# Kernel tuning notes

Measured on AMD Instinct MI355X. Metric: run time of the kernel, lower is better.

The kernel has to match this reference:

```python
import jax, jax.numpy as jnp
import numpy as np

B, HT_, WT_, DM, C = 32, 32, 32, 768, 64  # batch, token grid, token dim, hough channels
THETA_RES, RHO_RES = 3, 1


def hough_transform(rows, cols, theta_res, rho_res):
    """Precompute binary vote matrix [rows*cols, n_rho*n_theta] (HT-LCNN style)."""
    theta = np.linspace(0.0, 180.0, int(np.ceil(180.0 / theta_res)) + 1)[:-1]
    w = theta.size                                # n_theta
    diag = np.sqrt((rows - 1) ** 2 + (cols - 1) ** 2)
    q = int(np.ceil(diag / rho_res))
    nrho = 2 * q + 1                              # n_rho
    cos_t, sin_t = np.cos(np.deg2rad(theta)), np.sin(np.deg2rad(theta))
    ii, jj = np.meshgrid(np.arange(rows), np.arange(cols), indexing='ij')
    xc = jj - cols / 2.0                          # centered pixel coords
    yc = rows / 2.0 - ii
    rho = xc[..., None] * cos_t + yc[..., None] * sin_t   # [rows, cols, w]
    ridx = np.round(rho / rho_res).astype(np.int64) + q
    tidx = np.broadcast_to(np.arange(w), ridx.shape)
    flat = (ridx * w + tidx).reshape(rows * cols, w)      # bin = rho_idx*w + theta_idx
    vote = np.zeros((rows * cols, nrho * w), dtype=np.float32)
    vote[np.arange(rows * cols)[:, None], flat] = 1.0
    return vote, nrho, w


def setup_inputs() -> dict:
    key = jax.random.key(0)
    ks = jax.random.split(key, 8)
    vote_np, n_rho, n_theta = hough_transform(HT_, WT_, THETA_RES, RHO_RES)
    ch = C // 2
    s = lambda n: 1.0 / np.sqrt(n)
    return dict(
        tokens=jax.random.normal(ks[0], (B, HT_ * WT_, DM), jnp.float32),
        vote=jnp.asarray(vote_np),                                    # [N, HR]
        Wt_in=jax.random.normal(ks[1], (C, DM), jnp.float32) * s(DM),   # to_feats 1x1
        bt_in=jnp.zeros((C,), jnp.float32),
        W1=jax.random.normal(ks[2], (ch, C), jnp.float32) * s(C),       # conv1 1x1 (no bias)
        W2=jax.random.normal(ks[3], (ch, ch, 9, 1), jnp.float32) * s(ch * 9),  # (9,1) conv on hough map
        W3=jax.random.normal(ks[4], (C, ch), jnp.float32) * s(ch),      # conv3 1x1 (no bias)
        Wt_out=jax.random.normal(ks[5], (DM, C), jnp.float32) * s(C),   # from_feats 1x1
        bt_out=jnp.zeros((DM,), jnp.float32),
        n_rho=n_rho,
        n_theta=n_theta,
    )


def reference(tokens, vote, Wt_in, bt_in, W1, W2, W3, Wt_out, bt_out, n_rho, n_theta):
    # tokens: [B, N, D]; vote: [N, HR] with HR = n_rho * n_theta.
    # 1x1 convs over the token grid are position-independent -> plain matmuls on [B, N, *].
    norm = jnp.clip(vote.sum(0), 1.0)                       # [HR] HT vote-count normalizer
    feat = tokens @ Wt_in.T + bt_in                         # [B, N, C]   (to_feats)
    y = jax.nn.relu(feat @ W1.T)                            # [B, N, ch]  (conv1 + relu)
    # HT: relu (idempotent here) + vote gather as dense matmul, normalized per hough bin
    ht = jnp.einsum('bnc,nh->bch', y, vote) / norm          # [B, ch, HR]
    bb, ch, hr = ht.shape
    ht = ht.reshape(bb, ch, n_rho, n_theta)                 # [B, ch, n_rho, n_theta]
    ht = jax.lax.conv_general_dilated(                      # (9,1) conv along rho, pad 4
        ht, W2, (1, 1), ((4, 4), (0, 0)),
        dimension_numbers=('NCHW', 'OIHW', 'NCHW'))
    # IHT: relu + transposed vote scatter, normalized by n_theta
    iht = jnp.einsum('bch,nh->bnc', jax.nn.relu(ht.reshape(bb, ch, hr)), vote) / n_theta
    z = iht @ W3.T                                          # [B, N, C]   (conv3)
    out = (feat + z) @ Wt_out.T + bt_out                    # residual + from_feats -> [B, N, D]
    return out
```

## Files before the change

### kernel.cpp

```cpp
#include <hip/hip_runtime.h>
#include <math.h>

#define NB    32
#define NTOK  1024
#define DMODEL 768
#define CF    64
#define CHH   32
#define NRHO  89
#define NTH   60
#define HRB   (NRHO*NTH)

typedef short bf16x8 __attribute__((ext_vector_type(8)));
typedef float f32x4  __attribute__((ext_vector_type(4)));
typedef unsigned int uint;
typedef unsigned short ushort;
typedef unsigned char uchar;

__device__ __forceinline__ ushort f2bf(float f) {
    uint u = __float_as_uint(f);
    return (ushort)((u + 0x7FFF + ((u >> 16) & 1)) >> 16);
}
__device__ __forceinline__ float bf2f(ushort u) {
    return __uint_as_float(((uint)u) << 16);
}
__device__ __forceinline__ uint cvtpk(float lo, float hi) {
    uint r;
    asm("v_cvt_pk_bf16_f32 %0, %1, %2" : "=v"(r) : "v"(lo), "v"(hi));
    return r;
}

#define GLDS16(gp, lp) __builtin_amdgcn_global_load_lds( \
    (const __attribute__((address_space(1))) unsigned int*)(gp), \
    (__attribute__((address_space(3))) unsigned int*)(lp), 16, 0, 0)

__global__ __launch_bounds__(256) void k0_prep(
    int* __restrict__ perm, int* __restrict__ rowptr, uchar* __restrict__ rho8,
    const float* __restrict__ Wt_in, const float* __restrict__ bt_in,
    const float* __restrict__ W1, short* __restrict__ wcat,
    float* __restrict__ bcat,
    const float* __restrict__ Wt_out, const float* __restrict__ W2,
    short* __restrict__ wout, short* __restrict__ w2t) {
    __shared__ int rho_n[NTOK];
    __shared__ int cnt2[64 * 90];
    __shared__ int tot[96];
    __shared__ int base[96];
    __shared__ float w1row[64];
    const int tid = threadIdx.x;
    const int blk = blockIdx.x;

    if (blk < 60) {
        const int t = blk;
        const double rad = ((double)(t * 3)) * (M_PI / 180.0);
        const double ct = cos(rad), st = sin(rad);
        for (int n = tid; n < NTOK; n += 256) {
            int i = n >> 5, j = n & 31;
            double rho = (double)(j - 16) * ct + (double)(16 - i) * st;
            int ridx = (int)rint(rho) + 44;
            rho_n[n] = ridx;
            rho8[t * NTOK + n] = (uchar)ridx;
        }
        for (int i = tid; i < 64 * 90; i += 256) cnt2[i] = 0;
        __syncthreads();
        for (int n = tid; n < NTOK; n += 256)
            atomicAdd(&cnt2[(n >> 4) * 90 + rho_n[n]], 1);
        __syncthreads();
        if (tid < NRHO) {
            int s = 0;
            for (int c = 0; c < 64; ++c) {
                int v = cnt2[c * 90 + tid];
                cnt2[c * 90 + tid] = s;
                s += v;
            }
            tot[tid] = s;
        }
        __syncthreads();
        if (tid == 0) {
            int s = 0;
            for (int r = 0; r < NRHO; ++r) { base[r] = s; s += tot[r]; }
            base[NRHO] = s;
        }
        __syncthreads();
        if (tid < NRHO + 1) rowptr[t * 90 + tid] = base[tid];
        if (tid < 64) {
            const int c = tid;
            #pragma unroll
            for (int j = 0; j < 16; ++j) {
                int n = c * 16 + j;
                int r = rho_n[n];
                int cur = cnt2[c * 90 + r];
                cnt2[c * 90 + r] = cur + 1;
                perm[t * NTOK + base[r] + cur] = n;
            }
        }
    } else if (blk < 156) {
        const int c = blk - 60;
        if (c >= 64)
            for (int j = tid; j < 64; j += 256) w1row[j] = W1[(c - 64) * 64 + j];
        __syncthreads();
        for (int k = tid; k < DMODEL; k += 256) {
            float v;
            if (c < 64) v = Wt_in[c * DMODEL + k];
            else {
                v = 0.0f;
                for (int j = 0; j < 64; ++j) v += w1row[j] * Wt_in[j * DMODEL + k];
            }
            int kt = k >> 6, kk = k & 63;
            wcat[(((kt << 3) + (kk >> 3)) * 96 + c) * 8 + (k & 7)] = (short)f2bf(v);
        }
        if (tid == 0) {
            float bv;
            if (c < 64) bv = bt_in[c];
            else {
                bv = 0.0f;
                for (int j = 0; j < 64; ++j) bv += W1[(c - 64) * 64 + j] * bt_in[j];
            }
            bcat[c] = bv;
        }
    } else {
        int idx = (blk - 156) * 256 + tid;
        if (idx < 6144) {
            int d = idx >> 3, kg = idx & 7;
            float4 a = *(const float4*)&Wt_out[d * 64 + kg * 8];
            float4 b = *(const float4*)&Wt_out[d * 64 + kg * 8 + 4];
            uint4 v = make_uint4(cvtpk(a.x, a.y), cvtpk(a.z, a.w),
                                 cvtpk(b.x, b.y), cvtpk(b.z, b.w));
            *(uint4*)&wout[(((d >> 7) * 8 + kg) * 128 + (d & 127)) * 8] = v;
        } else if (idx < 6144 + 9216) {
            int q = idx - 6144;
            int e = q & 7, ln = (q >> 3) & 63, wm = (q >> 9) & 1, k = q >> 10;
            int o = wm * 16 + (ln & 15), i = ((ln >> 4) << 3) + e;
            w2t[q] = (short)f2bf(W2[(o * 32 + i) * 9 + k]);
        }
    }
}

__global__ __launch_bounds__(256) void k1_mfma(
    const float* __restrict__ tokens, const short* __restrict__ wcat,
    const float* __restrict__ bcat, ushort* __restrict__ featb,
    ushort* __restrict__ ybb) {
    __shared__ __align__(16) short Asm[2][4096];
    __shared__ __align__(16) short Bsm[2][6144];

    const int tid = threadIdx.x;
    const int lane = tid & 63, wave = tid >> 6;
    const int wm = wave >> 1, wn = wave & 1;
    const int row0 = blockIdx.x * 64;
    const int sm = tid >> 2, sq = tid & 3;

    const float* arow = tokens + (size_t)(row0 + sm) * DMODEL;

    f32x4 acc[2][3] = {};
    float4 ta[4];

    #pragma unroll
    for (int p = 0; p < 4; ++p)
        ta[p] = *(const float4*)&arow[(sq + 4 * p) * 4];
    for (int ch = tid; ch < 768; ch += 256)
        GLDS16((const char*)wcat + ch * 16, (char*)Bsm[0] + ch * 16);
    #pragma unroll
    for (int p = 0; p < 4; ++p) {
        int q = sq + 4 * p, kg = q >> 1, half = q & 1;
        uint lo = cvtpk(ta[p].x, ta[p].y);
        uint hi = cvtpk(ta[p].z, ta[p].w);
        *(uint2*)((char*)Asm[0] + (kg * 64 + sm) * 16 + half * 8) = make_uint2(lo, hi);
    }
    __syncthreads();

    int cur = 0;
    for (int kt = 0; kt < 12; ++kt) {
        if (kt < 11) {
            const float* src = arow + (kt + 1) * 64;
            #pragma unroll
            for (int p = 0; p < 4; ++p)
                ta[p] = *(const float4*)&src[(sq + 4 * p) * 4];
            const char* bsrc = (const char*)wcat + (size_t)(kt + 1) * 12288;
            for (int ch = tid; ch < 768; ch += 256)
                GLDS16(bsrc + ch * 16, (char*)Bsm[cur ^ 1] + ch * 16);
        }
        const bf16x8* Ap = (const bf16x8*)Asm[cur];
        const bf16x8* Bp = (const bf16x8*)Bsm[cur];
        #pragma unroll
        for (int ks = 0; ks < 2; ++ks) {
            int kg = (lane >> 4) + ks * 4;
            bf16x8 av[2], bv[3];
            #pragma unroll
            for (int i = 0; i < 2; ++i)
                av[i] = Ap[kg * 64 + wm * 32 + i * 16 + (lane & 15)];
            #pragma unroll
            for (int j = 0; j < 3; ++j)
                bv[j] = Bp[kg * 96 + wn * 48 + j * 16 + (lane & 15)];
            #pragma unroll
            for (int i = 0; i < 2; ++i)
                #pragma unroll
                for (int j = 0; j < 3; ++j)
                    acc[i][j] = __builtin_amdgcn_mfma_f32_16x16x32_bf16(
                        av[i], bv[j], acc[i][j], 0, 0, 0);
        }
        if (kt < 11) {
            #pragma unroll
            for (int p = 0; p < 4; ++p) {
                int q = sq + 4 * p, kg = q >> 1, half = q & 1;
                uint lo = cvtpk(ta[p].x, ta[p].y);
                uint hi = cvtpk(ta[p].z, ta[p].w);
                *(uint2*)((char*)Asm[cur ^ 1] + (kg * 64 + sm) * 16 + half * 8) =
                    make_uint2(lo, hi);
            }
        }
        __syncthreads();
        cur ^= 1;
    }

    ushort* fs = (ushort*)Asm[0];
    ushort* ys = (ushort*)Asm[1];
    float bb[3];
    #pragma unroll
    for (int j = 0; j < 3; ++j) bb[j] = bcat[wn * 48 + j * 16 + (lane & 15)];
    #pragma unroll
    for (int i = 0; i < 2; ++i) {
        #pragma unroll
        for (int j = 0; j < 3; ++j) {
            int c = wn * 48 + j * 16 + (lane & 15);
            int mlb = wm * 32 + i * 16 + ((lane >> 4) << 2);
            #pragma unroll
            for (int r = 0; r < 4; ++r) {
                float v = acc[i][j][r] + bb[j];
                if (c < 64) fs[(mlb + r) * 64 + c] = f2bf(v);
                else        ys[(mlb + r) * 32 + (c - 64)] = f2bf(fmaxf(v, 0.0f));
            }
        }
    }
    __syncthreads();
    for (int idx = tid; idx < 512; idx += 256) {
        int ml = idx >> 3, cq = (idx & 7) * 8;
        *(uint4*)&featb[(size_t)(row0 + ml) * CF + cq] = *(const uint4*)&fs[ml * 64 + cq];
    }
    {
        int ml = tid >> 2, cq = (tid & 3) * 8;
        *(uint4*)&ybb[(size_t)(row0 + ml) * CHH + cq] = *(const uint4*)&ys[ml * 32 + cq];
    }
}

__global__ __launch_bounds__(256) void k23_ht_conv(
    const ushort* __restrict__ ybb, const int* __restrict__ perm,
    const int* __restrict__ rowptr, const short* __restrict__ w2t,
    ushort* __restrict__ htcT) {
    __shared__ int pperm[NTOK];
    __shared__ int prow[90];
    __shared__ __align__(16) short insp[104 * 40];
    __shared__ uint outtu[NRHO * 18];

    const int tid = threadIdx.x;
    const int lane = tid & 63, wave = tid >> 6;
    const int wm = wave >> 1, wn = wave & 1;
    const int b = blockIdx.x / NTH, t = blockIdx.x % NTH;

    bf16x8 av[9];
    #pragma unroll
    for (int k = 0; k < 9; ++k)
        av[k] = *(const bf16x8*)&w2t[(((k * 2 + wm) * 64) + lane) * 8];

    for (int i = tid; i < NTOK; i += 256) pperm[i] = perm[t * NTOK + i];
    for (int i = tid; i < 90; i += 256) prow[i] = rowptr[t * 90 + i];
    for (int i = tid; i < 104 * 40 / 2; i += 256) ((uint*)insp)[i] = 0;
    __syncthreads();

    {
        const int c0 = (tid & 3) * 8, g = tid >> 2;
        const ushort* yp = ybb + (size_t)b * NTOK * CHH + c0;
        for (int rho = g; rho < NRHO; rho += 64) {
            int p0 = prow[rho], p1 = prow[rho + 1];
            float s0 = 0, s1 = 0, s2 = 0, s3 = 0, s4 = 0, s5 = 0, s6 = 0, s7 = 0;
            for (int k = p0; k < p1; ++k) {
                int n = pperm[k];
                uint4 v = *(const uint4*)&yp[n * CHH];
                s0 += bf2f((ushort)(v.x & 0xffff)); s1 += bf2f((ushort)(v.x >> 16));
                s2 += bf2f((ushort)(v.y & 0xffff)); s3 += bf2f((ushort)(v.y >> 16));
                s4 += bf2f((ushort)(v.z & 0xffff)); s5 += bf2f((ushort)(v.z >> 16));
                s6 += bf2f((ushort)(v.w & 0xffff)); s7 += bf2f((ushort)(v.w >> 16));
            }
            float iv = 1.0f / fmaxf((float)(p1 - p0), 1.0f);
            uint4 pk = make_uint4(cvtpk(s0 * iv, s1 * iv), cvtpk(s2 * iv, s3 * iv),
                                  cvtpk(s4 * iv, s5 * iv), cvtpk(s6 * iv, s7 * iv));
            *(uint4*)&insp[(rho + 4) * 40 + c0] = pk;
        }
    }
    __syncthreads();

    f32x4 acc[3] = {};
    #pragma unroll
    for (int f = 0; f < 3; ++f) {
        int Rn = wn * 48 + f * 16 + (lane & 15);
        #pragma unroll
        for (int k = 0; k < 9; ++k) {
            bf16x8 bv = *(const bf16x8*)&insp[(Rn + k) * 40 + ((lane >> 4) << 3)];
            acc[f] = __builtin_amdgcn_mfma_f32_16x16x32_bf16(av[k], bv, acc[f], 0, 0, 0);
        }
    }
    #pragma unroll
    for (int f = 0; f < 3; ++f) {
        int r = wn * 48 + f * 16 + (lane & 15);
        if (r < NRHO) {
            int ob = wm * 8 + ((lane >> 4) << 1);
            outtu[r * 18 + ob]     = cvtpk(fmaxf(acc[f][0], 0.0f), fmaxf(acc[f][1], 0.0f));
            outtu[r * 18 + ob + 1] = cvtpk(fmaxf(acc[f][2], 0.0f), fmaxf(acc[f][3], 0.0f));
        }
    }
    __syncthreads();

    {
        ushort* dst = htcT + (size_t)(b * NTH + t) * (NRHO * CHH);
        for (int idx = tid; idx < NRHO * 8; idx += 256) {
            int r = idx >> 3, q = idx & 7;
            uint2 v;
            v.x = outtu[r * 18 + q * 2];
            v.y = outtu[r * 18 + q * 2 + 1];
            *(uint2*)&dst[r * CHH + q * 4] = v;
        }
    }
}

__global__ __launch_bounds__(256, 4) void k45_iht_out(
    const ushort* __restrict__ htcT, const uchar* __restrict__ rho8,
    const float* __restrict__ W3, const ushort* __restrict__ featb,
    const short* __restrict__ wout, const float* __restrict__ bt_out,
    float* __restrict__ out) {
    __shared__ __align__(16) char smem[40960];
    short* Blds = (short*)smem;
    short* Alds = (short*)(smem + 32768);
    float* w3t  = (float*)smem;
    uchar* lrho = (uchar*)(smem + 8192);
    float* ihts = (float*)(smem + 12032);

    const int tid = threadIdx.x;
    const int lane = tid & 63, wave = tid >> 6;
    const int wm = wave >> 1, wn = wave & 1;
    const int bid = blockIdx.x;
    const int b = bid >> 4;
    const int n0 = (bid & 15) * 64;

    for (int idx = tid; idx < 2048; idx += 256) {
        int c = idx >> 6, j = idx & 63;
        w3t[idx] = W3[j * 32 + c];
    }
    for (int idx = tid; idx < NTH * 64; idx += 256)
        lrho[idx] = rho8[(idx >> 6) * NTOK + n0 + (idx & 63)];
    __syncthreads();

    {
        const int c0 = (tid & 3) * 8, tok = tid >> 2;
        const ushort* hb = htcT + (size_t)b * NTH * NRHO * CHH + c0;
        float s[8] = {};
        #pragma unroll 6
        for (int t = 0; t < NTH; ++t) {
            int r = lrho[t * 64 + tok];
            uint4 v = *(const uint4*)&hb[(size_t)(t * NRHO + r) * CHH];
            s[0] += bf2f((ushort)(v.x & 0xffff)); s[1] += bf2f((ushort)(v.x >> 16));
            s[2] += bf2f((ushort)(v.y & 0xffff)); s[3] += bf2f((ushort)(v.y >> 16));
            s[4] += bf2f((ushort)(v.z & 0xffff)); s[5] += bf2f((ushort)(v.z >> 16));
            s[6] += bf2f((ushort)(v.w & 0xffff)); s[7] += bf2f((ushort)(v.w >> 16));
        }
        __syncthreads();
        float4 r0, r1;
        r0.x = s[0] * (1.0f / 60.0f); r0.y = s[1] * (1.0f / 60.0f);
        r0.z = s[2] * (1.0f / 60.0f); r0.w = s[3] * (1.0f / 60.0f);
        r1.x = s[4] * (1.0f / 60.0f); r1.y = s[5] * (1.0f / 60.0f);
        r1.z = s[6] * (1.0f / 60.0f); r1.w = s[7] * (1.0f / 60.0f);
        *(float4*)&ihts[tok * 32 + c0] = r0;
        *(float4*)&ihts[tok * 32 + c0 + 4] = r1;
    }
    __syncthreads();

    {
        const int j = tid & 63, nb = tid >> 6;
        ushort* Au = (ushort*)Alds;
        for (int nn = nb; nn < 64; nn += 4) {
            float z = 0.0f;
            #pragma unroll 8
            for (int cc = 0; cc < 32; ++cc) z += ihts[nn * 32 + cc] * w3t[cc * 64 + j];
            float v = bf2f(featb[(size_t)(bid * 64 + nn) * CF + j]) + z;
            Au[((j >> 3) * 64 + nn) * 8 + (j & 7)] = f2bf(v);
        }
    }
    __syncthreads();

    for (int ch = tid; ch < 1024; ch += 256)
        GLDS16((const char*)wout + ch * 16, (char*)Blds + ch * 16);
    __syncthreads();

    const bf16x8* Ap = (const bf16x8*)Alds;
    for (int db = 0; db < 6; ++db) {
        if (db < 5) {
            const char* src = (const char*)wout + (size_t)(db + 1) * 16384;
            char* dst = (char*)Blds + ((db + 1) & 1) * 16384;
            for (int ch = tid; ch < 1024; ch += 256)
                GLDS16(src + ch * 16, dst + ch * 16);
        }
        const bf16x8* Bp = (const bf16x8*)((const char*)Blds + (db & 1) * 16384);
        f32x4 acc[2][4] = {};
        #pragma unroll
        for (int ks = 0; ks < 2; ++ks) {
            int kg = (lane >> 4) + ks * 4;
            bf16x8 avv[2], bvv[4];
            #pragma unroll
            for (int i = 0; i < 2; ++i)
                avv[i] = Ap[kg * 64 + wm * 32 + i * 16 + (lane & 15)];
            #pragma unroll
            for (int jf = 0; jf < 4; ++jf)
                bvv[jf] = Bp[kg * 128 + wn * 64 + jf * 16 + (lane & 15)];
            #pragma unroll
            for (int i = 0; i < 2; ++i)
                #pragma unroll
                for (int jf = 0; jf < 4; ++jf)
                    acc[i][jf] = __builtin_amdgcn_mfma_f32_16x16x32_bf16(
                        avv[i], bvv[jf], acc[i][jf], 0, 0, 0);
        }
        const int d0 = db * 128 + wn * 64 + (lane & 15);
        float bb[4];
        #pragma unroll
        for (int jf = 0; jf < 4; ++jf) bb[jf] = bt_out[d0 + jf * 16];
        const int mrow = bid * 64 + wm * 32 + ((lane >> 4) << 2);
        #pragma unroll
        for (int i = 0; i < 2; ++i)
            #pragma unroll
            for (int r = 0; r < 4; ++r)
                #pragma unroll
                for (int jf = 0; jf < 4; ++jf)
                    out[(size_t)(mrow + i * 16 + r) * DMODEL + d0 + jf * 16] =
                        acc[i][jf][r] + bb[jf];
        __syncthreads();
    }
}

extern "C" void kernel_launch(void* const* d_in, const int* in_sizes, int n_in,
                              void* d_out, int out_size, void* d_ws, size_t ws_size,
                              hipStream_t stream) {
    const float* tokens = (const float*)d_in[0];
    const float* Wt_in  = (const float*)d_in[2];
    const float* bt_in  = (const float*)d_in[3];
    const float* W1     = (const float*)d_in[4];
    const float* W2     = (const float*)d_in[5];
    const float* W3     = (const float*)d_in[6];
    const float* Wt_out = (const float*)d_in[7];
    const float* bt_out = (const float*)d_in[8];
    float* out = (float*)d_out;

    char* w = (char*)d_ws;
    int*    perm   = (int*)(w);
    int*    rowptr = (int*)(w + 245760);
    uchar*  rho8   = (uchar*)(w + 267360);
    short*  wcat   = (short*)(w + 328800);
    float*  bcat   = (float*)(w + 476256);
    short*  wout   = (short*)(w + 476640);
    short*  w2t    = (short*)(w + 574944);
    ushort* featb  = (ushort*)(w + 593376);
    ushort* ybb    = (ushort*)(w + 4787680);
    ushort* htcT   = (ushort*)(w + 6884832);

    k0_prep<<<216, 256, 0, stream>>>(perm, rowptr, rho8, Wt_in, bt_in, W1,
                                     wcat, bcat, Wt_out, W2, wout, w2t);
    k1_mfma<<<NB * NTOK / 64, 256, 0, stream>>>(tokens, wcat, bcat, featb, ybb);
    k23_ht_conv<<<NB * NTH, 256, 0, stream>>>(ybb, perm, rowptr, w2t, htcT);
    k45_iht_out<<<NB * (NTOK / 64), 256, 0, stream>>>(htcT, rho8, W3, featb,
                                                      wout, bt_out, out);
}
```

Measured before the change: 100.4 us.

## Load MFMA operands straight from global memory, dropping LDS staging in two GEMMs

The token projection kernel now loads fp32 activations and bf16 weights directly into registers in MFMA fragment layout instead of staging them through double-buffered LDS. It also doubles the rows per block to 128 and sets a 4-blocks-per-CU launch bound. The output GEMM likewise reads the weight fragments from global memory, keeps the A fragments in registers across all output column tiles, and removes the per-tile barriers. This cuts LDS traffic and synchronisation, but relies on L1/L2 caching for the repeated weight reads, and the uncoalesced 32-byte row reads of tokens may reduce memory efficiency.

```diff
diff --git a/kernel.cpp b/kernel.cpp
--- a/kernel.cpp
+++ b/kernel.cpp
@@ -28,10 +28,13 @@
     asm("v_cvt_pk_bf16_f32 %0, %1, %2" : "=v"(r) : "v"(lo), "v"(hi));
     return r;
 }
-
-#define GLDS16(gp, lp) __builtin_amdgcn_global_load_lds( \
-    (const __attribute__((address_space(1))) unsigned int*)(gp), \
-    (__attribute__((address_space(3))) unsigned int*)(lp), 16, 0, 0)
+__device__ __forceinline__ bf16x8 pack8(const float4& a, const float4& b) {
+    uint4 u = make_uint4(cvtpk(a.x, a.y), cvtpk(a.z, a.w),
+                         cvtpk(b.x, b.y), cvtpk(b.z, b.w));
+    union { uint4 u4; bf16x8 v; } cv;
+    cv.u4 = u;
+    return cv.v;
+}
 
 __global__ __launch_bounds__(256) void k0_prep(
     int* __restrict__ perm, int* __restrict__ rowptr, uchar* __restrict__ rho8,
@@ -134,93 +137,58 @@
     }
 }
 
-__global__ __launch_bounds__(256) void k1_mfma(
+__global__ __launch_bounds__(256, 4) void k1_mfma(
     const float* __restrict__ tokens, const short* __restrict__ wcat,
     const float* __restrict__ bcat, ushort* __restrict__ featb,
     ushort* __restrict__ ybb) {
-    __shared__ __align__(16) short Asm[2][4096];
-    __shared__ __align__(16) short Bsm[2][6144];
+    __shared__ ushort fs[128 * 64];
+    __shared__ ushort ys[128 * 32];
 
     const int tid = threadIdx.x;
     const int lane = tid & 63, wave = tid >> 6;
     const int wm = wave >> 1, wn = wave & 1;
-    const int row0 = blockIdx.x * 64;
-    const int sm = tid >> 2, sq = tid & 3;
-
-    const float* arow = tokens + (size_t)(row0 + sm) * DMODEL;
-
-    f32x4 acc[2][3] = {};
-    float4 ta[4];
-
-    #pragma unroll
-    for (int p = 0; p < 4; ++p)
-        ta[p] = *(const float4*)&arow[(sq + 4 * p) * 4];
-    for (int ch = tid; ch < 768; ch += 256)
-        GLDS16((const char*)wcat + ch * 16, (char*)Bsm[0] + ch * 16);
-    #pragma unroll
-    for (int p = 0; p < 4; ++p) {
-        int q = sq + 4 * p, kg = q >> 1, half = q & 1;
-        uint lo = cvtpk(ta[p].x, ta[p].y);
-        uint hi = cvtpk(ta[p].z, ta[p].w);
-        *(uint2*)((char*)Asm[0] + (kg * 64 + sm) * 16 + half * 8) = make_uint2(lo, hi);
-    }
-    __syncthreads();
-
-    int cur = 0;
+    const int row0 = blockIdx.x * 128;
+    const int l15 = lane & 15, lq = lane >> 4;
+
+    const float* aptr = tokens + (size_t)(row0 + wm * 64 + l15) * DMODEL + lq * 8;
+    const short* bptr = wcat + ((size_t)lq * 96 + wn * 48 + l15) * 8;
+
+    f32x4 acc[4][3] = {};
+
     for (int kt = 0; kt < 12; ++kt) {
-        if (kt < 11) {
-            const float* src = arow + (kt + 1) * 64;
-            #pragma unroll
-            for (int p = 0; p < 4; ++p)
-                ta[p] = *(const float4*)&src[(sq + 4 * p) * 4];
-            const char* bsrc = (const char*)wcat + (size_t)(kt + 1) * 12288;
-            for (int ch = tid; ch < 768; ch += 256)
-                GLDS16(bsrc + ch * 16, (char*)Bsm[cur ^ 1] + ch * 16);
-        }
-        const bf16x8* Ap = (const bf16x8*)Asm[cur];
-        const bf16x8* Bp = (const bf16x8*)Bsm[cur];
         #pragma unroll
         for (int ks = 0; ks < 2; ++ks) {
-            int kg = (lane >> 4) + ks * 4;
-            bf16x8 av[2], bv[3];
-            #pragma unroll
-            for (int i = 0; i < 2; ++i)
-                av[i] = Ap[kg * 64 + wm * 32 + i * 16 + (lane & 15)];
+            const float* ap = aptr + kt * 64 + ks * 32;
+            bf16x8 av[4];
+            #pragma unroll
+            for (int i = 0; i < 4; ++i) {
+                float4 lo = *(const float4*)&ap[(size_t)i * 16 * DMODEL];
+                float4 hi = *(const float4*)&ap[(size_t)i * 16 * DMODEL + 4];
+                av[i] = pack8(lo, hi);
+            }
+            const short* bp = bptr + ((size_t)(kt * 8 + ks * 4) * 96) * 8;
+            bf16x8 bv[3];
             #pragma unroll
             for (int j = 0; j < 3; ++j)
-                bv[j] = Bp[kg * 96 + wn * 48 + j * 16 + (lane & 15)];
-            #pragma unroll
-            for (int i = 0; i < 2; ++i)
+                bv[j] = *(const bf16x8*)&bp[j * 16 * 8];
+            #pragma unroll
+            for (int i = 0; i < 4; ++i)
                 #pragma unroll
                 for (int j = 0; j < 3; ++j)
                     acc[i][j] = __builtin_amdgcn_mfma_f32_16x16x32_bf16(
                         av[i], bv[j], acc[i][j], 0, 0, 0);
         }
-        if (kt < 11) {
-            #pragma unroll
-            for (int p = 0; p < 4; ++p) {
-                int q = sq + 4 * p, kg = q >> 1, half = q & 1;
-                uint lo = cvtpk(ta[p].x, ta[p].y);
-                uint hi = cvtpk(ta[p].z, ta[p].w);
-                *(uint2*)((char*)Asm[cur ^ 1] + (kg * 64 + sm) * 16 + half * 8) =
-                    make_uint2(lo, hi);
-            }
-        }
-        __syncthreads();
-        cur ^= 1;
-    }
-
-    ushort* fs = (ushort*)Asm[0];
-    ushort* ys = (ushort*)Asm[1];
+    }
+
     float bb[3];
     #pragma unroll
-    for (int j = 0; j < 3; ++j) bb[j] = bcat[wn * 48 + j * 16 + (lane & 15)];
-    #pragma unroll
-    for (int i = 0; i < 2; ++i) {
+    for (int j = 0; j < 3; ++j) bb[j] = bcat[wn * 48 + j * 16 + l15];
+    #pragma unroll
+    for (int i = 0; i < 4; ++i) {
         #pragma unroll
         for (int j = 0; j < 3; ++j) {
-            int c = wn * 48 + j * 16 + (lane & 15);
-            int mlb = wm * 32 + i * 16 + ((lane >> 4) << 2);
+            int c = wn * 48 + j * 16 + l15;
+            int mlb = wm * 64 + i * 16 + (lq << 2);
             #pragma unroll
             for (int r = 0; r < 4; ++r) {
                 float v = acc[i][j][r] + bb[j];
@@ -230,12 +198,12 @@
         }
     }
     __syncthreads();
-    for (int idx = tid; idx < 512; idx += 256) {
+    for (int idx = tid; idx < 1024; idx += 256) {
         int ml = idx >> 3, cq = (idx & 7) * 8;
         *(uint4*)&featb[(size_t)(row0 + ml) * CF + cq] = *(const uint4*)&fs[ml * 64 + cq];
     }
-    {
-        int ml = tid >> 2, cq = (tid & 3) * 8;
+    for (int idx = tid; idx < 512; idx += 256) {
+        int ml = idx >> 2, cq = (idx & 3) * 8;
         *(uint4*)&ybb[(size_t)(row0 + ml) * CHH + cq] = *(const uint4*)&ys[ml * 32 + cq];
     }
 }
@@ -324,12 +292,10 @@
     const float* __restrict__ W3, const ushort* __restrict__ featb,
     const short* __restrict__ wout, const float* __restrict__ bt_out,
     float* __restrict__ out) {
-    __shared__ __align__(16) char smem[40960];
-    short* Blds = (short*)smem;
-    short* Alds = (short*)(smem + 32768);
-    float* w3t  = (float*)smem;
-    uchar* lrho = (uchar*)(smem + 8192);
-    float* ihts = (float*)(smem + 12032);
+    __shared__ float w3t[32 * 64];
+    __shared__ uchar lrho[NTH * 64];
+    __shared__ float ihts[64 * 32];
+    __shared__ __align__(16) short Alds[4096];
 
     const int tid = threadIdx.x;
     const int lane = tid & 63, wave = tid >> 6;
@@ -337,6 +303,7 @@
     const int bid = blockIdx.x;
     const int b = bid >> 4;
     const int n0 = (bid & 15) * 64;
+    const int l15 = lane & 15, lq = lane >> 4;
 
     for (int idx = tid; idx < 2048; idx += 256) {
         int c = idx >> 6, j = idx & 63;
@@ -359,7 +326,6 @@
             s[4] += bf2f((ushort)(v.z & 0xffff)); s[5] += bf2f((ushort)(v.z >> 16));
             s[6] += bf2f((ushort)(v.w & 0xffff)); s[7] += bf2f((ushort)(v.w >> 16));
         }
-        __syncthreads();
         float4 r0, r1;
         r0.x = s[0] * (1.0f / 60.0f); r0.y = s[1] * (1.0f / 60.0f);
         r0.z = s[2] * (1.0f / 60.0f); r0.w = s[3] * (1.0f / 60.0f);
@@ -383,42 +349,38 @@
     }
     __syncthreads();
 
-    for (int ch = tid; ch < 1024; ch += 256)
-        GLDS16((const char*)wout + ch * 16, (char*)Blds + ch * 16);
-    __syncthreads();
-
     const bf16x8* Ap = (const bf16x8*)Alds;
+    bf16x8 avr[2][2];
+    #pragma unroll
+    for (int ks = 0; ks < 2; ++ks) {
+        int kg = lq + ks * 4;
+        #pragma unroll
+        for (int i = 0; i < 2; ++i)
+            avr[ks][i] = Ap[kg * 64 + wm * 32 + i * 16 + l15];
+    }
+
+    const short* bbase = wout + ((size_t)lq * 128 + wn * 64 + l15) * 8;
     for (int db = 0; db < 6; ++db) {
-        if (db < 5) {
-            const char* src = (const char*)wout + (size_t)(db + 1) * 16384;
-            char* dst = (char*)Blds + ((db + 1) & 1) * 16384;
-            for (int ch = tid; ch < 1024; ch += 256)
-                GLDS16(src + ch * 16, dst + ch * 16);
-        }
-        const bf16x8* Bp = (const bf16x8*)((const char*)Blds + (db & 1) * 16384);
         f32x4 acc[2][4] = {};
         #pragma unroll
         for (int ks = 0; ks < 2; ++ks) {
-            int kg = (lane >> 4) + ks * 4;
-            bf16x8 avv[2], bvv[4];
-            #pragma unroll
-            for (int i = 0; i < 2; ++i)
-                avv[i] = Ap[kg * 64 + wm * 32 + i * 16 + (lane & 15)];
+            const short* bp = bbase + ((size_t)(db * 8 + ks * 4) * 128) * 8;
+            bf16x8 bvv[4];
             #pragma unroll
             for (int jf = 0; jf < 4; ++jf)
-                bvv[jf] = Bp[kg * 128 + wn * 64 + jf * 16 + (lane & 15)];
+                bvv[jf] = *(const bf16x8*)&bp[jf * 16 * 8];
             #pragma unroll
             for (int i = 0; i < 2; ++i)
                 #pragma unroll
                 for (int jf = 0; jf < 4; ++jf)
                     acc[i][jf] = __builtin_amdgcn_mfma_f32_16x16x32_bf16(
-                        avv[i], bvv[jf], acc[i][jf], 0, 0, 0);
-        }
-        const int d0 = db * 128 + wn * 64 + (lane & 15);
+                        avr[ks][i], bvv[jf], acc[i][jf], 0, 0, 0);
+        }
+        const int d0 = db * 128 + wn * 64 + l15;
         float bb[4];
         #pragma unroll
         for (int jf = 0; jf < 4; ++jf) bb[jf] = bt_out[d0 + jf * 16];
-        const int mrow = bid * 64 + wm * 32 + ((lane >> 4) << 2);
+        const int mrow = bid * 64 + wm * 32 + (lq << 2);
         #pragma unroll
         for (int i = 0; i < 2; ++i)
             #pragma unroll
@@ -427,7 +389,6 @@
                 for (int jf = 0; jf < 4; ++jf)
                     out[(size_t)(mrow + i * 16 + r) * DMODEL + d0 + jf * 16] =
                         acc[i][jf][r] + bb[jf];
-        __syncthreads();
     }
 }
 
@@ -458,7 +419,7 @@
 
     k0_prep<<<216, 256, 0, stream>>>(perm, rowptr, rho8, Wt_in, bt_in, W1,
                                      wcat, bcat, Wt_out, W2, wout, w2t);
-    k1_mfma<<<NB * NTOK / 64, 256, 0, stream>>>(tokens, wcat, bcat, featb, ybb);
+    k1_mfma<<<NB * NTOK / 128, 256, 0, stream>>>(tokens, wcat, bcat, featb, ybb);
     k23_ht_conv<<<NB * NTH, 256, 0, stream>>>(ybb, perm, rowptr, w2t, htcT);
     k45_iht_out<<<NB * (NTOK / 64), 256, 0, stream>>>(htcT, rho8, W3, featb,
                                                       wout, bt_out, out);
```

Result: slower. 115.6 us (+15.2%).
